# Kernel optimization log

Measured on AMD Instinct MI355X. Metric: run time of the kernel, lower is better.

Reference implementation:

```python
import jax, jax.numpy as jnp
import numpy as np

B, N, C, H = 8, 1024, 1024, 16
D = C // H
SCALE = D ** -0.5


def setup_inputs() -> dict:
    key = jax.random.key(0)
    ks = jax.random.split(key, 5)
    s = 0.02  # keep pre-softmax logits in a sane range
    return {
        "x": jax.random.normal(ks[0], (B, N, C), dtype=jnp.float32),
        "Wq": jax.random.normal(ks[1], (C, C), dtype=jnp.float32) * s,
        "bq": jax.random.normal(ks[2], (C,), dtype=jnp.float32) * s,
        "Wkv": jax.random.normal(ks[3], (C, 2 * C), dtype=jnp.float32) * s,
        "bkv": jax.random.normal(ks[4], (2 * C,), dtype=jnp.float32) * s,
    }


def reference(x, Wq, bq, Wkv, bkv):
    b, n, c = x.shape
    h, d = H, c // H
    q = (x @ Wq + bq).reshape(b, n, h, d)                 # [b,n,h,d]
    kv = x @ Wkv + bkv                                     # [b,n,2c]
    k, v = jnp.split(kv, 2, axis=-1)                       # each [b,n,c]
    k = k.reshape(b, n, h, d)
    v = v.reshape(b, n, h, d)
    att = jnp.einsum("bnhd,bmhd->bnmh", q, k) * SCALE      # [b,n,m,h]
    att = jax.nn.softmax(att, axis=2)                      # softmax over keys (m)
    out = jnp.einsum("bnmh,bmhd->bnhd", att, v).reshape(b, n, c)
    return out
```

## Files before the change

### kernel.cpp

```cpp
#include <hip/hip_runtime.h>
#include <stdint.h>

using u16 = unsigned short;
using u32 = unsigned int;
using bf16x8 = __attribute__((ext_vector_type(8))) __bf16;
using f32x4  = __attribute__((ext_vector_type(4))) float;

#define NB 8
#define NN 1024
#define NC 1024
#define NH 16
#define ND 64
#define QSCALE 0.18033688011112042f

__device__ __forceinline__ u16 f2bf(float f) {
  u32 u = __float_as_uint(f);
  return (u16)((u + 0x7fffu + ((u >> 16) & 1u)) >> 16);
}
__device__ __forceinline__ u16 bfc(float f) {
  __bf16 b = (__bf16)f;
  return __builtin_bit_cast(u16, b);
}
__device__ __forceinline__ u32 pack2(u16 a, u16 b) { return (u32)a | ((u32)b << 16); }

__device__ __forceinline__ void gload16(const void* g, void* l) {
  __builtin_amdgcn_global_load_lds((__attribute__((address_space(1))) const u32*)g,
                                   (__attribute__((address_space(3))) u32*)l, 16, 0, 0);
}

__global__ void k_prep(const float* __restrict__ x, const float* __restrict__ Wq,
                       const float* __restrict__ Wkv,
                       u16* __restrict__ xb, u16* __restrict__ Wt) {
  __shared__ u16 tile[64][72];
  int bid = blockIdx.x;
  int t = threadIdx.x;
  if (bid < 8192) {
    int i = bid * 256 + t;
    float4 v = ((const float4*)x)[i];
    ((uint2*)xb)[i] = make_uint2(pack2(f2bf(v.x), f2bf(v.y)), pack2(f2bf(v.z), f2bf(v.w)));
    return;
  }
  {
    int pb = bid - 8192;
    int k0 = (pb & 15) << 6;
    int c0 = (pb >> 4) << 6;
    bool isQ = (c0 < 1024);
    const float* src = isQ ? Wq : Wkv;
    int ldw  = isQ ? 1024 : 2048;
    int csrc = isQ ? c0 : (c0 - 1024);
    float sc = isQ ? QSCALE : 1.0f;

    int r  = t >> 2;
    int cq = (t & 3) << 4;
    const float* p = src + (size_t)(k0 + r) * ldw + csrc + cq;
#pragma unroll
    for (int j = 0; j < 16; j += 4) {
      float4 v = *(const float4*)(p + j);
      tile[r][cq + j + 0] = f2bf(v.x * sc);
      tile[r][cq + j + 1] = f2bf(v.y * sc);
      tile[r][cq + j + 2] = f2bf(v.z * sc);
      tile[r][cq + j + 3] = f2bf(v.w * sc);
    }
    __syncthreads();
    int co = t >> 2;
    int kq = (t & 3) << 4;
    u16 v0[16];
#pragma unroll
    for (int j = 0; j < 16; ++j) v0[j] = tile[kq + j][co];
    uint4 o0, o1;
    o0.x = pack2(v0[0], v0[1]);  o0.y = pack2(v0[2], v0[3]);
    o0.z = pack2(v0[4], v0[5]);  o0.w = pack2(v0[6], v0[7]);
    o1.x = pack2(v0[8], v0[9]);  o1.y = pack2(v0[10], v0[11]);
    o1.z = pack2(v0[12], v0[13]); o1.w = pack2(v0[14], v0[15]);
    u16* dst = Wt + (size_t)(c0 + co) * 1024 + k0 + kq;
    *(uint4*)dst = o0;
    *(uint4*)(dst + 8) = o1;
  }
}

__launch_bounds__(512, 2)
__global__ void k_gemm(const u16* __restrict__ A, const u16* __restrict__ Bw,
                       const float* __restrict__ bq, const float* __restrict__ bkv,
                       u16* __restrict__ qws, u16* __restrict__ kws, u16* __restrict__ vtw) {
  __shared__ __align__(16) u16 LA[2][16384];
  __shared__ __align__(16) u16 LB[2][24576];
  int flat = blockIdx.x;
  int xcd = flat & 7, idx = flat >> 3;
  int m0 = (xcd * 4 + (idx & 3)) * 256;
  int n0 = (idx >> 2) * 384;
  int tid = threadIdx.x;
  int w = tid >> 6, lane = tid & 63;
  int lo = lane & 15, hi = lane >> 4;
  int wm = w >> 2, wn = w & 3;

  f32x4 acc[8][6] = {};

  int cs = ((tid & 7) ^ ((tid >> 3) & 7)) * 8;
  const u16* Ag = A  + (size_t)(m0 + (tid >> 3)) * 1024 + cs;
  const u16* Bg = Bw + (size_t)(n0 + (tid >> 3)) * 1024 + cs;

  int ck0 = ((hi ^ (lo & 7)) << 3);
  int ck1 = (((4 + hi) ^ (lo & 7)) << 3);
  const u16* laR = &LA[0][(wm * 128 + lo) * 64];
  const u16* lbR = &LB[0][(wn * 96 + lo) * 64];

#define MFMA_(a, b, c) __builtin_amdgcn_mfma_f32_16x16x32_bf16(a, b, c, 0, 0, 0)
#define SBAR() __builtin_amdgcn_sched_barrier(0); __builtin_amdgcn_s_barrier(); __builtin_amdgcn_sched_barrier(0)
#define LGKM0() asm volatile("s_waitcnt lgkmcnt(0)" ::: "memory"); __builtin_amdgcn_sched_barrier(0)

#define ST_A(BUF, P, KT) gload16(Ag + (size_t)((P) * 64) * 1024 + (KT) * 64, &LA[BUF][(P) * 4096 + tid * 8]);
#define ST_B(BUF, P, KT) gload16(Bg + (size_t)((P) * 64) * 1024 + (KT) * 64, &LB[BUF][(P) * 4096 + tid * 8]);

  ST_A(0, 0, 0); ST_A(0, 1, 0); ST_A(0, 2, 0); ST_A(0, 3, 0);
  ST_B(0, 0, 0); ST_B(0, 1, 0); ST_B(0, 2, 0); ST_B(0, 3, 0); ST_B(0, 4, 0); ST_B(0, 5, 0);
  asm volatile("s_waitcnt vmcnt(0)" ::: "memory");
  __builtin_amdgcn_s_barrier();

#pragma unroll 1
  for (int t = 0; t < 16; ++t) {
    int b = t & 1;
    const u16* la = laR + b * 16384;
    const u16* lb = lbR + b * 24576;
    bool st = (t < 15);
    int kn = t + 1;

#pragma unroll
    for (int q = 0; q < 2; ++q) {
      bf16x8 af[4][2];
#pragma unroll
      for (int mi = 0; mi < 4; ++mi) {
        af[mi][0] = *(const bf16x8*)(la + (q * 64 + mi * 16) * 64 + ck0);
        af[mi][1] = *(const bf16x8*)(la + (q * 64 + mi * 16) * 64 + ck1);
      }
#pragma unroll
      for (int ni = 0; ni < 6; ++ni) {
        bf16x8 bfr0 = *(const bf16x8*)(lb + ni * 1024 + ck0);
        bf16x8 bfr1 = *(const bf16x8*)(lb + ni * 1024 + ck1);
        if (st) {
          if (q == 0 && ni >= 1 && ni <= 4) { ST_A(b ^ 1, ni - 1, kn); }
          else if (q == 0 && ni == 5)       { ST_B(b ^ 1, 0, kn); }
          else if (q == 1 && ni <= 4)       { ST_B(b ^ 1, ni + 1, kn); }
        }
        SBAR();
        LGKM0();
        __builtin_amdgcn_s_setprio(1);
#pragma unroll
        for (int mi = 0; mi < 4; ++mi) {
          acc[q * 4 + mi][ni] = MFMA_(af[mi][0], bfr0, acc[q * 4 + mi][ni]);
          acc[q * 4 + mi][ni] = MFMA_(af[mi][1], bfr1, acc[q * 4 + mi][ni]);
        }
        __builtin_amdgcn_s_setprio(0);
        if (q == 1 && ni == 5) {
          if (st) { asm volatile("s_waitcnt vmcnt(0)" ::: "memory"); }
        }
        SBAR();
      }
    }
  }
#undef ST_A
#undef ST_B
#undef SBAR
#undef LGKM0
#undef MFMA_

#pragma unroll
  for (int ni = 0; ni < 6; ++ni) {
    int c = n0 + wn * 96 + ni * 16 + lo;
    float bvl = (c < 1024) ? bq[c] * QSCALE : bkv[c - 1024];
    if (c < 2048) {
#pragma unroll
      for (int mi = 0; mi < 8; ++mi) {
#pragma unroll
        for (int r = 0; r < 4; ++r) {
          int m = m0 + wm * 128 + mi * 16 + hi * 4 + r;
          int b = m >> 10, tok = m & 1023;
          u16 o = f2bf(acc[mi][ni][r] + bvl);
          if (c < 1024) {
            int h = c >> 6, d = c & 63;
            qws[((size_t)(b * 16 + h) * 1024 + tok) * 64 + d] = o;
          } else {
            int c2 = c - 1024; int h = c2 >> 6, d = c2 & 63;
            kws[((size_t)(b * 16 + h) * 1024 + tok) * 64 + d] = o;
          }
        }
      }
    } else {
      int c2 = c - 2048; int h = c2 >> 6, d = c2 & 63;
#pragma unroll
      for (int mi = 0; mi < 8; ++mi) {
        int m = m0 + wm * 128 + mi * 16 + hi * 4;
        int b = m >> 10, tok = m & 1023;
        ushort4 pk;
        pk.x = bfc(acc[mi][ni][0] + bvl);
        pk.y = bfc(acc[mi][ni][1] + bvl);
        pk.z = bfc(acc[mi][ni][2] + bvl);
        pk.w = bfc(acc[mi][ni][3] + bvl);
        *(ushort4*)&vtw[((size_t)(b * 16 + h) * 64 + d) * 1024 + tok] = pk;
      }
    }
  }
}

__launch_bounds__(512)
__global__ void k_attn(const u16* __restrict__ q, const u16* __restrict__ k,
                       const u16* __restrict__ vt, float* __restrict__ out) {
  __shared__ __align__(16) u16 Ks[2][4096];
  __shared__ __align__(16) u16 Vs[2][4096];
  __shared__ __align__(16) u16 P[2][8][16][72];
  int bh = blockIdx.x;
  int q0 = blockIdx.y * 256;
  int tid = threadIdx.x;
  int w = tid >> 6, lane = tid & 63;
  int lo = lane & 15, hi = lane >> 4;
  int b = bh >> 4, h = bh & 15;

  const u16* kbase = k  + (size_t)bh * 65536;
  const u16* vbase = vt + (size_t)bh * 65536;

  int srow = w * 8 + (lane >> 3);
  int cg   = (lane & 7) ^ ((lane >> 3) & 7);
  const u16* gK = kbase + (size_t)srow * 64   + cg * 8;
  const u16* gV = vbase + (size_t)srow * 1024 + cg * 8;
  u16* lK0 = &Ks[0][w * 512];
  u16* lK1 = &Ks[1][w * 512];
  u16* lV0 = &Vs[0][w * 512];
  u16* lV1 = &Vs[1][w * 512];

  const u16* qp = q + ((size_t)bh * 1024 + q0 + w * 16 + lo) * 64 + hi * 8;
  bf16x8 qfA0 = *(const bf16x8*)(qp);
  bf16x8 qfA1 = *(const bf16x8*)(qp + 32);
  bf16x8 qfB0 = *(const bf16x8*)(qp + 128 * 64);
  bf16x8 qfB1 = *(const bf16x8*)(qp + 128 * 64 + 32);

  f32x4 accA[4] = {}, accB[4] = {};
  float mA = -1e30f, lA = 0.f;
  float mB = -1e30f, lB = 0.f;

  int sw = lo & 7;

  gload16(gK, lK0);
  gload16(gV, lV0);
  __syncthreads();

  for (int t = 0; t < 16; ++t) {
    int cur = t & 1;
    if (t < 15) {
      gload16(gK + (t + 1) * 4096, cur ? lK0 : lK1);
      gload16(gV + (t + 1) * 64,   cur ? lV0 : lV1);
    }
    f32x4 sA[4] = {}, sB[4] = {};
    const u16* kb = Ks[cur];
    __builtin_amdgcn_s_setprio(1);
#pragma unroll
    for (int ni = 0; ni < 4; ++ni) {
      const u16* kp = kb + (ni * 16 + lo) * 64;
      bf16x8 kf0 = *(const bf16x8*)(kp + ((hi ^ sw) * 8));
      bf16x8 kf1 = *(const bf16x8*)(kp + (((4 + hi) ^ sw) * 8));
      sA[ni] = __builtin_amdgcn_mfma_f32_16x16x32_bf16(kf0, qfA0, sA[ni], 0, 0, 0);
      sA[ni] = __builtin_amdgcn_mfma_f32_16x16x32_bf16(kf1, qfA1, sA[ni], 0, 0, 0);
      sB[ni] = __builtin_amdgcn_mfma_f32_16x16x32_bf16(kf0, qfB0, sB[ni], 0, 0, 0);
      sB[ni] = __builtin_amdgcn_mfma_f32_16x16x32_bf16(kf1, qfB1, sB[ni], 0, 0, 0);
    }
    __builtin_amdgcn_s_setprio(0);

#define SOFTMAX(S, M, L, PI)                                                   \
    {                                                                          \
      float a0 = fmaxf(fmaxf(S[0][0], S[0][1]), fmaxf(S[0][2], S[0][3]));      \
      float a1 = fmaxf(fmaxf(S[1][0], S[1][1]), fmaxf(S[1][2], S[1][3]));      \
      float a2 = fmaxf(fmaxf(S[2][0], S[2][1]), fmaxf(S[2][2], S[2][3]));      \
      float a3 = fmaxf(fmaxf(S[3][0], S[3][1]), fmaxf(S[3][2], S[3][3]));      \
      float pm = fmaxf(fmaxf(a0, a1), fmaxf(a2, a3));                          \
      pm = fmaxf(pm, __shfl_xor(pm, 16));                                      \
      pm = fmaxf(pm, __shfl_xor(pm, 32));                                      \
      if (!__all(pm <= M + 8.0f)) {                                            \
        float mn = fmaxf(M, pm);                                               \
        float corr = __builtin_amdgcn_exp2f(M - mn);                           \
        M = mn;                                                                \
        L *= corr;                                                             \
        float cr[4];                                                           \
        _Pragma("unroll")                                                      \
        for (int r = 0; r < 4; ++r) cr[r] = __shfl(corr, hi * 4 + r);          \
        _Pragma("unroll")                                                      \
        for (int ci = 0; ci < 4; ++ci)                                         \
          _Pragma("unroll")                                                    \
          for (int r = 0; r < 4; ++r) acc##PI[ci][r] *= cr[r];                 \
      }                                                                        \
      float rs = 0.f;                                                          \
      _Pragma("unroll")                                                        \
      for (int ni = 0; ni < 4; ++ni) {                                         \
        float p0 = __builtin_amdgcn_exp2f(S[ni][0] - M);                       \
        float p1 = __builtin_amdgcn_exp2f(S[ni][1] - M);                       \
        float p2 = __builtin_amdgcn_exp2f(S[ni][2] - M);                       \
        float p3 = __builtin_amdgcn_exp2f(S[ni][3] - M);                       \
        rs += (p0 + p1) + (p2 + p3);                                           \
        ushort4 pk;                                                            \
        pk.x = bfc(p0); pk.y = bfc(p1); pk.z = bfc(p2); pk.w = bfc(p3);        \
        *(ushort4*)&P[PI##I][w][lo][ni * 16 + hi * 4] = pk;                    \
      }                                                                        \
      rs += __shfl_xor(rs, 16);                                                \
      rs += __shfl_xor(rs, 32);                                                \
      L += rs;                                                                 \
    }
#define AI 0
#define BI 1
    SOFTMAX(sA, mA, lA, A)
    SOFTMAX(sB, mB, lB, B)
#undef SOFTMAX

    bf16x8 pA0 = *(const bf16x8*)(&P[0][w][lo][hi * 8]);
    bf16x8 pA1 = *(const bf16x8*)(&P[0][w][lo][32 + hi * 8]);
    bf16x8 pB0 = *(const bf16x8*)(&P[1][w][lo][hi * 8]);
    bf16x8 pB1 = *(const bf16x8*)(&P[1][w][lo][32 + hi * 8]);
    const u16* vb = Vs[cur];
    __builtin_amdgcn_s_setprio(1);
#pragma unroll
    for (int ci = 0; ci < 4; ++ci) {
      const u16* vp = vb + (ci * 16 + lo) * 64;
      bf16x8 vf0 = *(const bf16x8*)(vp + ((hi ^ sw) * 8));
      bf16x8 vf1 = *(const bf16x8*)(vp + (((4 + hi) ^ sw) * 8));
      accA[ci] = __builtin_amdgcn_mfma_f32_16x16x32_bf16(pA0, vf0, accA[ci], 0, 0, 0);
      accA[ci] = __builtin_amdgcn_mfma_f32_16x16x32_bf16(pA1, vf1, accA[ci], 0, 0, 0);
      accB[ci] = __builtin_amdgcn_mfma_f32_16x16x32_bf16(pB0, vf0, accB[ci], 0, 0, 0);
      accB[ci] = __builtin_amdgcn_mfma_f32_16x16x32_bf16(pB1, vf1, accB[ci], 0, 0, 0);
    }
    __builtin_amdgcn_s_setprio(0);
    __syncthreads();
  }
  {
    float inv = 1.0f / lA;
    float ivr[4];
#pragma unroll
    for (int r = 0; r < 4; ++r) ivr[r] = __shfl(inv, hi * 4 + r);
#pragma unroll
    for (int r = 0; r < 4; ++r) {
      int n = q0 + w * 16 + hi * 4 + r;
      float* dst = out + ((size_t)(b * 1024 + n)) * 1024 + h * 64;
#pragma unroll
      for (int ci = 0; ci < 4; ++ci) dst[ci * 16 + lo] = accA[ci][r] * ivr[r];
    }
  }
  {
    float inv = 1.0f / lB;
    float ivr[4];
#pragma unroll
    for (int r = 0; r < 4; ++r) ivr[r] = __shfl(inv, hi * 4 + r);
#pragma unroll
    for (int r = 0; r < 4; ++r) {
      int n = q0 + 128 + w * 16 + hi * 4 + r;
      float* dst = out + ((size_t)(b * 1024 + n)) * 1024 + h * 64;
#pragma unroll
      for (int ci = 0; ci < 4; ++ci) dst[ci * 16 + lo] = accB[ci][r] * ivr[r];
    }
  }
}

extern "C" void kernel_launch(void* const* d_in, const int* in_sizes, int n_in,
                              void* d_out, int out_size, void* d_ws, size_t ws_size,
                              hipStream_t stream) {
  const float* x   = (const float*)d_in[0];
  const float* Wq  = (const float*)d_in[1];
  const float* bq  = (const float*)d_in[2];
  const float* Wkv = (const float*)d_in[3];
  const float* bkv = (const float*)d_in[4];
  float* out = (float*)d_out;

  char* ws = (char*)d_ws;
  u16*   xb   = (u16*)(ws);
  u16*   Wt   = (u16*)(ws + 16777216);
  u16*   qws  = (u16*)(ws + 23080960);
  u16*   kws  = (u16*)(ws + 39858176);
  u16*   vtw  = (u16*)(ws + 73412608);

  k_prep<<<8960, 256, 0, stream>>>(x, Wq, Wkv, xb, Wt);
  k_gemm<<<256, 512, 0, stream>>>(xb, Wt, bq, bkv, qws, kws, vtw);
  {
    dim3 g(128, 4);
    k_attn<<<g, 512, 0, stream>>>(qws, kws, vtw, out);
  }
}
```

Measured before the change: 131.3 us.

## Issue whole next-tile prefetch upfront and drop per-step barriers in GEMM loop

Replaces the fine-grained interleaving of global->LDS loads with MFMA sub-steps (each step guarded by two barriers and an lgkmcnt wait) with one batch of all next-tile loads at the start of each k iteration. All B fragments are preloaded into registers and the MFMAs run without intermediate barriers. A single vmcnt/lgkmcnt wait plus barrier ends each iteration. This removes most sync overhead but leaves load/compute overlap to the hardware and compiler scheduling, and raises register pressure.

```diff
diff --git a/kernel.cpp b/kernel.cpp
--- a/kernel.cpp
+++ b/kernel.cpp
@@ -105,14 +105,14 @@
   const u16* lbR = &LB[0][(wn * 96 + lo) * 64];
 
 #define MFMA_(a, b, c) __builtin_amdgcn_mfma_f32_16x16x32_bf16(a, b, c, 0, 0, 0)
-#define SBAR() __builtin_amdgcn_sched_barrier(0); __builtin_amdgcn_s_barrier(); __builtin_amdgcn_sched_barrier(0)
-#define LGKM0() asm volatile("s_waitcnt lgkmcnt(0)" ::: "memory"); __builtin_amdgcn_sched_barrier(0)
-
 #define ST_A(BUF, P, KT) gload16(Ag + (size_t)((P) * 64) * 1024 + (KT) * 64, &LA[BUF][(P) * 4096 + tid * 8]);
 #define ST_B(BUF, P, KT) gload16(Bg + (size_t)((P) * 64) * 1024 + (KT) * 64, &LB[BUF][(P) * 4096 + tid * 8]);
-
-  ST_A(0, 0, 0); ST_A(0, 1, 0); ST_A(0, 2, 0); ST_A(0, 3, 0);
-  ST_B(0, 0, 0); ST_B(0, 1, 0); ST_B(0, 2, 0); ST_B(0, 3, 0); ST_B(0, 4, 0); ST_B(0, 5, 0);
+#define ST_TILE(BUF, KT)                                                     \
+  ST_A(BUF, 0, KT); ST_A(BUF, 1, KT); ST_A(BUF, 2, KT); ST_A(BUF, 3, KT);    \
+  ST_B(BUF, 0, KT); ST_B(BUF, 1, KT); ST_B(BUF, 2, KT);                      \
+  ST_B(BUF, 3, KT); ST_B(BUF, 4, KT); ST_B(BUF, 5, KT);
+
+  ST_TILE(0, 0);
   asm volatile("s_waitcnt vmcnt(0)" ::: "memory");
   __builtin_amdgcn_s_barrier();
 
@@ -121,9 +121,16 @@
     int b = t & 1;
     const u16* la = laR + b * 16384;
     const u16* lb = lbR + b * 24576;
-    bool st = (t < 15);
-    int kn = t + 1;
-
+
+    if (t < 15) { ST_TILE(b ^ 1, t + 1); }
+    __builtin_amdgcn_sched_barrier(0);
+
+    bf16x8 bfr[6][2];
+#pragma unroll
+    for (int ni = 0; ni < 6; ++ni) {
+      bfr[ni][0] = *(const bf16x8*)(lb + ni * 1024 + ck0);
+      bfr[ni][1] = *(const bf16x8*)(lb + ni * 1024 + ck1);
+    }
 #pragma unroll
     for (int q = 0; q < 2; ++q) {
       bf16x8 af[4][2];
@@ -133,34 +140,22 @@
         af[mi][1] = *(const bf16x8*)(la + (q * 64 + mi * 16) * 64 + ck1);
       }
 #pragma unroll
-      for (int ni = 0; ni < 6; ++ni) {
-        bf16x8 bfr0 = *(const bf16x8*)(lb + ni * 1024 + ck0);
-        bf16x8 bfr1 = *(const bf16x8*)(lb + ni * 1024 + ck1);
-        if (st) {
-          if (q == 0 && ni >= 1 && ni <= 4) { ST_A(b ^ 1, ni - 1, kn); }
-          else if (q == 0 && ni == 5)       { ST_B(b ^ 1, 0, kn); }
-          else if (q == 1 && ni <= 4)       { ST_B(b ^ 1, ni + 1, kn); }
+      for (int ni = 0; ni < 6; ++ni)
+#pragma unroll
+        for (int mi = 0; mi < 4; ++mi) {
+          acc[q * 4 + mi][ni] = MFMA_(af[mi][0], bfr[ni][0], acc[q * 4 + mi][ni]);
+          acc[q * 4 + mi][ni] = MFMA_(af[mi][1], bfr[ni][1], acc[q * 4 + mi][ni]);
         }
-        SBAR();
-        LGKM0();
-        __builtin_amdgcn_s_setprio(1);
-#pragma unroll
-        for (int mi = 0; mi < 4; ++mi) {
-          acc[q * 4 + mi][ni] = MFMA_(af[mi][0], bfr0, acc[q * 4 + mi][ni]);
-          acc[q * 4 + mi][ni] = MFMA_(af[mi][1], bfr1, acc[q * 4 + mi][ni]);
-        }
-        __builtin_amdgcn_s_setprio(0);
-        if (q == 1 && ni == 5) {
-          if (st) { asm volatile("s_waitcnt vmcnt(0)" ::: "memory"); }
-        }
-        SBAR();
-      }
-    }
-  }
+    }
+
+    if (t < 15) {
+      asm volatile("s_waitcnt vmcnt(0) lgkmcnt(0)" ::: "memory");
+      __builtin_amdgcn_s_barrier();
+    }
+  }
+#undef ST_TILE
 #undef ST_A
 #undef ST_B
-#undef SBAR
-#undef LGKM0
 #undef MFMA_
 
 #pragma unroll
```

Result: slower. 143.0 us (+8.9%).
